# Performance work log

Hardware: AMD Instinct MI355X
Metric: run time of the kernel (lower is better)

## Reference

```python
import jax, jax.numpy as jnp
import numpy as np

B, HASHLEN, D = 65536, 64, 300


def setup_inputs() -> dict:
    key = jax.random.key(0)
    k = jax.random.split(key, 7)
    return {
        "b": jax.random.normal(k[0], (B, HASHLEN), dtype=jnp.float32),
        "labels": jax.random.randint(k[1], (B,), 0, 100, dtype=jnp.int64),
        "Wmu": jax.random.normal(k[2], (HASHLEN, D), dtype=jnp.float32) * 0.05,
        "bmu": jax.random.normal(k[3], (D,), dtype=jnp.float32) * 0.05,
        "Wsig": jax.random.normal(k[4], (HASHLEN, D), dtype=jnp.float32) * 0.05,
        "bsig": jax.random.normal(k[5], (D,), dtype=jnp.float32) * 0.05,
        "eps": jax.random.normal(k[6], (B, D), dtype=jnp.float32),
    }


def reference(b, labels, Wmu, bmu, Wsig, bsig, eps):
    # mean = mu(b); s = sigma(b); var = s*s
    mean = b @ Wmu + bmu            # [B, 300]
    s = b @ Wsig + bsig             # [B, 300]
    var = s * s                     # [B, 300]
    # MVN with covariance diag(var): cholesky(diag(var)) = diag(sqrt(var)),
    # so rsample = mean + sqrt(var) * eps (elementwise; no dense 300x300 cov).
    sample = mean + jnp.sqrt(var) * eps
    return sample, mean, var
```

## Files before the change

### kernel.cpp

```cpp
#include <hip/hip_runtime.h>
#include <hip/hip_bf16.h>


#define B_ROWS 65536
#define K_DIM 64
#define D_DIM 300
#define NFRAG 19
#define ROWS_PER_BLOCK 64
#define THREADS 512
#define QPR 75
#define QPB (ROWS_PER_BLOCK * QPR)
#define EPQ 10

typedef __fp16 half2v __attribute__((ext_vector_type(2)));
typedef __fp16 half8v __attribute__((ext_vector_type(8)));
typedef float  f32x4  __attribute__((ext_vector_type(4)));
typedef unsigned int u32x4 __attribute__((ext_vector_type(4)));

__device__ __forceinline__ half2v h2(unsigned int u) {
    return __builtin_bit_cast(half2v, u);
}
__device__ __forceinline__ unsigned int pkd(float a, float b) {
    return __builtin_bit_cast(unsigned int, __builtin_amdgcn_cvt_pkrtz(a, b));
}
__device__ __forceinline__ half8v pack8(float4 x, float4 y) {
    half2v p0 = __builtin_amdgcn_cvt_pkrtz(x.x, x.y);
    half2v p1 = __builtin_amdgcn_cvt_pkrtz(x.z, x.w);
    half2v p2 = __builtin_amdgcn_cvt_pkrtz(y.x, y.y);
    half2v p3 = __builtin_amdgcn_cvt_pkrtz(y.z, y.w);
    half8v r;
    r[0] = p0[0]; r[1] = p0[1]; r[2] = p1[0]; r[3] = p1[1];
    r[4] = p2[0]; r[5] = p2[1]; r[6] = p3[0]; r[7] = p3[1];
    return r;
}

__global__ void pack_w_kernel(const float* __restrict__ Wmu,
                              const float* __restrict__ Wsig,
                              half8v* __restrict__ wpack)
{
    const int t = blockIdx.x * blockDim.x + threadIdx.x;
    const int total = 2 * NFRAG * 2 * 64;
    if (t >= total) return;
    const int lane = t & 63;
    const int fs   = t >> 6;
    const int s    = fs & 1;
    const int mf   = fs >> 1;
    const int m    = mf / NFRAG;
    const int f    = mf - m * NFRAG;
    const int col  = f * 16 + (lane & 15);
    const int k0   = s * 32 + (lane >> 4) * 8;
    const float* W = m ? Wsig : Wmu;
    half8v o;
    #pragma unroll
    for (int e = 0; e < 8; ++e) {
        float v = (col < D_DIM) ? W[(size_t)(k0 + e) * D_DIM + col] : 0.f;
        o[e] = (__fp16)v;
    }
    wpack[t] = o;
}

__global__ __launch_bounds__(THREADS, 2) void sem_dec_main(
    const float* __restrict__ b,
    const float* __restrict__ bmu,
    const float* __restrict__ bsig,
    const float* __restrict__ eps,
    const half8v* __restrict__ wpack,
    float* __restrict__ out)
{
    __shared__ unsigned int lds_ms[ROWS_PER_BLOCK * D_DIM];

    const int tid  = threadIdx.x;
    const int lane = tid & 63;
    const int wid  = tid >> 6;
    const int row0 = blockIdx.x * ROWS_PER_BLOCK;

    const size_t gq0 = (size_t)row0 * QPR;
    const f32x4* eps4 = reinterpret_cast<const f32x4*>(eps);
    f32x4 epr[EPQ];
    #pragma unroll
    for (int i = 0; i < EPQ; ++i) {
        const int q = tid + i * THREADS;
        if (q < QPB) epr[i] = __builtin_nontemporal_load(&eps4[gq0 + q]);
    }

    const int arow = lane & 15;
    const int kg   = lane >> 4;
    half8v a0[4], a1[4];
    #pragma unroll
    for (int rt = 0; rt < 4; ++rt) {
        const float* bp = b + (size_t)(row0 + rt * 16 + arow) * K_DIM + kg * 8;
        float4 v0 = *reinterpret_cast<const float4*>(bp);
        float4 v1 = *reinterpret_cast<const float4*>(bp + 4);
        float4 v2 = *reinterpret_cast<const float4*>(bp + 32);
        float4 v3 = *reinterpret_cast<const float4*>(bp + 36);
        a0[rt] = pack8(v0, v1);
        a1[rt] = pack8(v2, v3);
    }

    const int ccol = lane & 15;
    const int crow = (lane >> 4) * 4;

    #pragma unroll
    for (int fi = 0; fi < 3; ++fi) {
        const int f = wid + fi * 8;
        if (f >= NFRAG) break;
        const int c = f * 16 + ccol;
        const bool cval = (c < D_DIM);
        half8v wm0 = wpack[((0 * NFRAG + f) * 2 + 0) * 64 + lane];
        half8v wm1 = wpack[((0 * NFRAG + f) * 2 + 1) * 64 + lane];
        half8v ws0 = wpack[((1 * NFRAG + f) * 2 + 0) * 64 + lane];
        half8v ws1 = wpack[((1 * NFRAG + f) * 2 + 1) * 64 + lane];
        const float biasm = cval ? bmu[c] : 0.f;
        const float biass = cval ? bsig[c] : 0.f;
        #pragma unroll
        for (int rt = 0; rt < 4; ++rt) {
            f32x4 accm = {biasm, biasm, biasm, biasm};
            f32x4 accs = {biass, biass, biass, biass};
            accm = __builtin_amdgcn_mfma_f32_16x16x32_f16(a0[rt], wm0, accm, 0, 0, 0);
            accm = __builtin_amdgcn_mfma_f32_16x16x32_f16(a1[rt], wm1, accm, 0, 0, 0);
            accs = __builtin_amdgcn_mfma_f32_16x16x32_f16(a0[rt], ws0, accs, 0, 0, 0);
            accs = __builtin_amdgcn_mfma_f32_16x16x32_f16(a1[rt], ws1, accs, 0, 0, 0);
            if (cval) {
                #pragma unroll
                for (int r = 0; r < 4; ++r)
                    lds_ms[(rt * 16 + crow + r) * D_DIM + c] =
                        pkd(accm[r], accs[r]);
            }
        }
    }
    __syncthreads();

    const size_t BD = (size_t)B_ROWS * D_DIM;
    f32x4* samp4 = reinterpret_cast<f32x4*>(out);
    f32x4* mean4 = reinterpret_cast<f32x4*>(out + BD);
    f32x4* var4  = reinterpret_cast<f32x4*>(out + 2 * BD);
    const u32x4* lds4 = reinterpret_cast<const u32x4*>(lds_ms);
    #pragma unroll
    for (int i = 0; i < EPQ; ++i) {
        const int q = tid + i * THREADS;
        if (q < QPB) {
            const u32x4 ms = lds4[q];
            const f32x4 e = epr[i];
            const half2v p0 = h2(ms.x), p1 = h2(ms.y);
            const half2v p2 = h2(ms.z), p3 = h2(ms.w);
            f32x4 mv, sv, sm, vr;
            mv.x = (float)p0[0]; sv.x = (float)p0[1];
            mv.y = (float)p1[0]; sv.y = (float)p1[1];
            mv.z = (float)p2[0]; sv.z = (float)p2[1];
            mv.w = (float)p3[0]; sv.w = (float)p3[1];
            sm.x = fmaf(fabsf(sv.x), e.x, mv.x);  vr.x = sv.x * sv.x;
            sm.y = fmaf(fabsf(sv.y), e.y, mv.y);  vr.y = sv.y * sv.y;
            sm.z = fmaf(fabsf(sv.z), e.z, mv.z);  vr.z = sv.z * sv.z;
            sm.w = fmaf(fabsf(sv.w), e.w, mv.w);  vr.w = sv.w * sv.w;
            __builtin_nontemporal_store(sm, &samp4[gq0 + q]);
            __builtin_nontemporal_store(mv, &mean4[gq0 + q]);
            __builtin_nontemporal_store(vr, &var4[gq0 + q]);
        }
    }
}

extern "C" void kernel_launch(void* const* d_in, const int* in_sizes, int n_in,
                              void* d_out, int out_size, void* d_ws, size_t ws_size,
                              hipStream_t stream) {
    const float* b    = (const float*)d_in[0];
    const float* Wmu  = (const float*)d_in[2];
    const float* bmu  = (const float*)d_in[3];
    const float* Wsig = (const float*)d_in[4];
    const float* bsig = (const float*)d_in[5];
    const float* eps  = (const float*)d_in[6];
    float* out = (float*)d_out;
    half8v* wpack = (half8v*)d_ws;

    hipLaunchKernelGGL(pack_w_kernel, dim3(19), dim3(256), 0, stream,
                       Wmu, Wsig, wpack);
    hipLaunchKernelGGL(sem_dec_main, dim3(B_ROWS / ROWS_PER_BLOCK),
                       dim3(THREADS), 0, stream,
                       b, bmu, bsig, eps, wpack, out);
}
```

Baseline: 72.55 us.

## Split block into two row halves to overlap epilogue stores with MFMA compute

Each 64-row block is now processed as two 32-row halves. The eps loads for the second half are issued, and the first half's epilogue stores run, before the second half's MFMA compute. The aim is to overlap global memory traffic with compute and lower peak register use for eps buffers. The cost is an extra barrier and a more serialized schedule, plus weights and bias reloaded for each half.

After: 77.17 us. +6.4%, slower.

```diff
diff --git a/kernel.cpp b/kernel.cpp
--- a/kernel.cpp
+++ b/kernel.cpp
@@ -7,10 +7,11 @@
 #define D_DIM 300
 #define NFRAG 19
 #define ROWS_PER_BLOCK 64
+#define HROWS 32
 #define THREADS 512
 #define QPR 75
-#define QPB (ROWS_PER_BLOCK * QPR)
-#define EPQ 10
+#define QPH (HROWS * QPR)
+#define EPQ_H 5
 
 typedef __fp16 half2v __attribute__((ext_vector_type(2)));
 typedef __fp16 half8v __attribute__((ext_vector_type(8)));
@@ -59,36 +60,21 @@
     wpack[t] = o;
 }
 
-__global__ __launch_bounds__(THREADS, 2) void sem_dec_main(
+__device__ __forceinline__ void compute_half(
+    int h, int row0, int lane, int wid,
     const float* __restrict__ b,
     const float* __restrict__ bmu,
     const float* __restrict__ bsig,
-    const float* __restrict__ eps,
     const half8v* __restrict__ wpack,
-    float* __restrict__ out)
-{
-    __shared__ unsigned int lds_ms[ROWS_PER_BLOCK * D_DIM];
-
-    const int tid  = threadIdx.x;
-    const int lane = tid & 63;
-    const int wid  = tid >> 6;
-    const int row0 = blockIdx.x * ROWS_PER_BLOCK;
-
-    const size_t gq0 = (size_t)row0 * QPR;
-    const f32x4* eps4 = reinterpret_cast<const f32x4*>(eps);
-    f32x4 epr[EPQ];
-    #pragma unroll
-    for (int i = 0; i < EPQ; ++i) {
-        const int q = tid + i * THREADS;
-        if (q < QPB) epr[i] = __builtin_nontemporal_load(&eps4[gq0 + q]);
-    }
-
+    unsigned int* __restrict__ lds_ms)
+{
     const int arow = lane & 15;
     const int kg   = lane >> 4;
-    half8v a0[4], a1[4];
-    #pragma unroll
-    for (int rt = 0; rt < 4; ++rt) {
-        const float* bp = b + (size_t)(row0 + rt * 16 + arow) * K_DIM + kg * 8;
+    half8v a0[2], a1[2];
+    #pragma unroll
+    for (int rt = 0; rt < 2; ++rt) {
+        const float* bp =
+            b + (size_t)(row0 + h * HROWS + rt * 16 + arow) * K_DIM + kg * 8;
         float4 v0 = *reinterpret_cast<const float4*>(bp);
         float4 v1 = *reinterpret_cast<const float4*>(bp + 4);
         float4 v2 = *reinterpret_cast<const float4*>(bp + 32);
@@ -96,10 +82,8 @@
         a0[rt] = pack8(v0, v1);
         a1[rt] = pack8(v2, v3);
     }
-
     const int ccol = lane & 15;
     const int crow = (lane >> 4) * 4;
-
     #pragma unroll
     for (int fi = 0; fi < 3; ++fi) {
         const int f = wid + fi * 8;
@@ -113,7 +97,7 @@
         const float biasm = cval ? bmu[c] : 0.f;
         const float biass = cval ? bsig[c] : 0.f;
         #pragma unroll
-        for (int rt = 0; rt < 4; ++rt) {
+        for (int rt = 0; rt < 2; ++rt) {
             f32x4 accm = {biasm, biasm, biasm, biasm};
             f32x4 accs = {biass, biass, biass, biass};
             accm = __builtin_amdgcn_mfma_f32_16x16x32_f16(a0[rt], wm0, accm, 0, 0, 0);
@@ -123,23 +107,28 @@
             if (cval) {
                 #pragma unroll
                 for (int r = 0; r < 4; ++r)
-                    lds_ms[(rt * 16 + crow + r) * D_DIM + c] =
+                    lds_ms[(h * HROWS + rt * 16 + crow + r) * D_DIM + c] =
                         pkd(accm[r], accs[r]);
             }
         }
     }
-    __syncthreads();
-
+}
+
+__device__ __forceinline__ void epilogue_half(
+    int h, int tid, size_t gq0, const f32x4* epr,
+    const unsigned int* __restrict__ lds_ms, float* __restrict__ out)
+{
     const size_t BD = (size_t)B_ROWS * D_DIM;
     f32x4* samp4 = reinterpret_cast<f32x4*>(out);
     f32x4* mean4 = reinterpret_cast<f32x4*>(out + BD);
     f32x4* var4  = reinterpret_cast<f32x4*>(out + 2 * BD);
     const u32x4* lds4 = reinterpret_cast<const u32x4*>(lds_ms);
     #pragma unroll
-    for (int i = 0; i < EPQ; ++i) {
+    for (int i = 0; i < EPQ_H; ++i) {
         const int q = tid + i * THREADS;
-        if (q < QPB) {
-            const u32x4 ms = lds4[q];
+        if (q < QPH) {
+            const int qb = h * QPH + q;
+            const u32x4 ms = lds4[qb];
             const f32x4 e = epr[i];
             const half2v p0 = h2(ms.x), p1 = h2(ms.y);
             const half2v p2 = h2(ms.z), p3 = h2(ms.w);
@@ -152,11 +141,54 @@
             sm.y = fmaf(fabsf(sv.y), e.y, mv.y);  vr.y = sv.y * sv.y;
             sm.z = fmaf(fabsf(sv.z), e.z, mv.z);  vr.z = sv.z * sv.z;
             sm.w = fmaf(fabsf(sv.w), e.w, mv.w);  vr.w = sv.w * sv.w;
-            __builtin_nontemporal_store(sm, &samp4[gq0 + q]);
-            __builtin_nontemporal_store(mv, &mean4[gq0 + q]);
-            __builtin_nontemporal_store(vr, &var4[gq0 + q]);
+            __builtin_nontemporal_store(sm, &samp4[gq0 + qb]);
+            __builtin_nontemporal_store(mv, &mean4[gq0 + qb]);
+            __builtin_nontemporal_store(vr, &var4[gq0 + qb]);
         }
     }
+}
+
+__global__ __launch_bounds__(THREADS, 2) void sem_dec_main(
+    const float* __restrict__ b,
+    const float* __restrict__ bmu,
+    const float* __restrict__ bsig,
+    const float* __restrict__ eps,
+    const half8v* __restrict__ wpack,
+    float* __restrict__ out)
+{
+    __shared__ unsigned int lds_ms[ROWS_PER_BLOCK * D_DIM];
+
+    const int tid  = threadIdx.x;
+    const int lane = tid & 63;
+    const int wid  = tid >> 6;
+    const int row0 = blockIdx.x * ROWS_PER_BLOCK;
+    const size_t gq0 = (size_t)row0 * QPR;
+    const f32x4* eps4 = reinterpret_cast<const f32x4*>(eps);
+
+    f32x4 epr0[EPQ_H];
+    #pragma unroll
+    for (int i = 0; i < EPQ_H; ++i) {
+        const int q = tid + i * THREADS;
+        if (q < QPH) epr0[i] = __builtin_nontemporal_load(&eps4[gq0 + q]);
+    }
+    compute_half(0, row0, lane, wid, b, bmu, bsig, wpack, lds_ms);
+
+    __syncthreads();
+
+    f32x4 epr1[EPQ_H];
+    #pragma unroll
+    for (int i = 0; i < EPQ_H; ++i) {
+        const int q = tid + i * THREADS;
+        if (q < QPH) epr1[i] = __builtin_nontemporal_load(&eps4[gq0 + QPH + q]);
+    }
+    epilogue_half(0, tid, gq0, epr0, lds_ms, out);
+    compute_half(1, row0, lane, wid, b, bmu, bsig, wpack, lds_ms);
+
+    asm volatile("s_waitcnt lgkmcnt(0)" ::: "memory");
+    __builtin_amdgcn_s_barrier();
+    __builtin_amdgcn_sched_barrier(0);
+
+    epilogue_half(1, tid, gq0, epr1, lds_ms, out);
 }
 
 extern "C" void kernel_launch(void* const* d_in, const int* in_sizes, int n_in,
```
